# Performance work log

Measured on AMD Instinct MI355X. Metric: run time of the kernel, lower is better.

The kernel has to match this reference:

```python
import jax, jax.numpy as jnp
import numpy as np

GAMMA = 1.0

def _rbf_mean(a, b, gamma):
    # mean of exp(-gamma * ||a_i - b_j||^2) over the full [Na, Nb] kernel matrix
    aa = jnp.sum(a * a, axis=1, keepdims=True)          # [Na, 1]
    bb = jnp.sum(b * b, axis=1, keepdims=True)          # [Nb, 1]
    dist = aa + bb.T - 2.0 * (a @ b.T)                  # [Na, Nb]
    return jnp.mean(jnp.exp(-gamma * dist))

def setup_inputs() -> dict:
    key = jax.random.key(0)
    kx, ky = jax.random.split(key)
    N, D = 8192, 128
    x = jax.random.normal(kx, (N, D), dtype=jnp.float32)
    y = jax.random.normal(ky, (N, D), dtype=jnp.float32)
    return {"x": x, "y": y}

def reference(x, y):
    mmd = (_rbf_mean(x, x, GAMMA)
           + _rbf_mean(y, y, GAMMA)
           - 2.0 * _rbf_mean(x, y, GAMMA))
    return mmd
```

## Files before the change

### kernel.cpp

```cpp
#include <hip/hip_runtime.h>


#define N_PTS 8192
#define DCOLS 128
#define TILE 128
#define TJ 64
#define NSELF 2080
#define NJOBS 8256
#define NBLOCKS 512
#define LOG2E 1.4426950408889634f
#define THRESH -40.0f

typedef __attribute__((ext_vector_type(8))) short short8;
typedef __attribute__((ext_vector_type(4))) float floatx4;
typedef unsigned int u32;
typedef unsigned short u16;

#if __has_builtin(__builtin_amdgcn_exp2f)
#define EXP2(x) __builtin_amdgcn_exp2f(x)
#else
#define EXP2(x) exp2f(x)
#endif

__device__ __forceinline__ u16 f32_to_bf16(float f) {
  u32 u = __float_as_uint(f);
  u32 r = (u + 0x7fffu + ((u >> 16) & 1u)) >> 16;
  return (u16)r;
}

__device__ __forceinline__ void gl_lds16(const u16* g, u16* l) {
  __builtin_amdgcn_global_load_lds(
      (const __attribute__((address_space(1))) u32*)g,
      (__attribute__((address_space(3))) u32*)l, 16, 0, 0);
}

__global__ void prep_kernel(const float* __restrict__ x, const float* __restrict__ y,
                            u32* __restrict__ xb, u32* __restrict__ yb,
                            float* __restrict__ da, float* __restrict__ db,
                            u32* __restrict__ Sz) {
  if (blockIdx.x == 0 && threadIdx.x < 4) Sz[threadIdx.x] = 0;
  int wid = threadIdx.x >> 6;
  int lane = threadIdx.x & 63;
  int row = blockIdx.x * 4 + wid;
  const float* src;
  u32* dst;
  float* dn;
  int r;
  if (row < N_PTS) { src = x; dst = xb; dn = da; r = row; }
  else             { src = y; dst = yb; dn = db; r = row - N_PTS; }
  float2 v = ((const float2*)(src + (size_t)r * DCOLS))[lane];
  u16 b0 = f32_to_bf16(v.x), b1 = f32_to_bf16(v.y);
  float f0 = __uint_as_float((u32)b0 << 16);
  float f1 = __uint_as_float((u32)b1 << 16);
  float p = f0 * f0 + f1 * f1;
  dst[(size_t)r * 64 + lane] = (u32)b0 | ((u32)b1 << 16);
#pragma unroll
  for (int off = 32; off; off >>= 1) p += __shfl_down(p, off, 64);
  if (lane == 0) dn[r] = -LOG2E * p;
}

struct Job { int pair, rr, cc; };

__device__ __forceinline__ Job decode_job(int t) {
  Job jb;
  if (t < 2 * NSELF) {
    jb.pair = (t < NSELF) ? 0 : 1;
    int tt = t - jb.pair * NSELF;
    int r = 0;
    while (tt >= TJ - r) { tt -= TJ - r; r++; }
    jb.rr = r; jb.cc = r + tt;
  } else {
    int q = t - 2 * NSELF;
    jb.pair = 2; jb.rr = q >> 6; jb.cc = q & 63;
  }
  return jb;
}

__device__ __forceinline__ Job next_job(Job c) {
  Job n = c;
  if (c.pair == 2) {
    if (c.cc == 63) { n.rr++; n.cc = 0; } else n.cc++;
  } else {
    if (c.cc == 63) {
      if (c.rr == 63) { n.pair++; n.rr = 0; n.cc = 0; }
      else { n.rr++; n.cc = n.rr; }
    } else n.cc++;
  }
  return n;
}

__device__ __forceinline__ void pair_ptrs(int pair, const u16* xb, const u16* yb,
                                          const float* da, const float* db,
                                          const u16*& A, const u16*& B,
                                          const float*& dA, const float*& dB) {
  A = (pair == 1) ? yb : xb;
  B = (pair == 0) ? xb : yb;
  dA = (pair == 1) ? db : da;
  dB = (pair == 0) ? da : db;
}

__device__ __forceinline__ void stage_tile(const u16* gsrc, u16* ldst,
                                           int wid, int quad, int l15) {
#pragma unroll
  for (int i = 0; i < 8; i++) {
    int ch = wid * 8 + i;
    int lrow = ch * 4 + quad;
    int bsw = l15 ^ (lrow & 15);
    gl_lds16(gsrc + lrow * DCOLS + bsw * 8, ldst + ch * 512);
  }
}

__device__ __forceinline__ void load_afrags(const u16* gA, const float* gdA, int rr,
                                            int mbase, int quad, int l15,
                                            short8 afr[4][4], float dam[16]) {
  const u16* base = gA + (size_t)rr * (TILE * DCOLS);
#pragma unroll
  for (int ks = 0; ks < 4; ks++)
#pragma unroll
    for (int mi = 0; mi < 4; mi++)
      afr[ks][mi] = *(const short8*)(base + (mbase + mi * 16 + l15) * DCOLS +
                                     ks * 32 + quad * 8);
  const float* dr = gdA + rr * TILE + mbase;
#pragma unroll
  for (int mi = 0; mi < 4; mi++)
#pragma unroll
    for (int v = 0; v < 4; v++) dam[mi * 4 + v] = dr[mi * 16 + quad * 4 + v];
}

__global__ __launch_bounds__(256, 2) void mmd_kernel(
    const u16* __restrict__ xb, const u16* __restrict__ yb,
    const float* __restrict__ da, const float* __restrict__ db,
    float* __restrict__ S, u32* __restrict__ cnt, float* __restrict__ out) {
  __shared__ u16 Bt[2][TILE * DCOLS];

  int tid = threadIdx.x;
  int wid = tid >> 6, lane = tid & 63;
  int quad = lane >> 4, l15 = lane & 15;
  int mbase = (wid >> 1) * 64, nbase = (wid & 1) * 64;

  int start = (blockIdx.x * NJOBS) >> 9;
  int end = ((blockIdx.x + 1) * NJOBS) >> 9;

  Job cur = decode_job(start);
  const u16 *cA, *cB;
  const float *cdA, *cdB;
  pair_ptrs(cur.pair, xb, yb, da, db, cA, cB, cdA, cdB);

  short8 afr[4][4];
  float dam[16];
  load_afrags(cA, cdA, cur.rr, mbase, quad, l15, afr, dam);
  stage_tile(cB + (size_t)cur.cc * (TILE * DCOLS), &Bt[0][0], wid, quad, l15);
  __syncthreads();

  const float c1 = 2.0f * LOG2E;
  float tsum = 0.f;
  int p = 0;

  for (int j = start; j < end; j++) {
    bool hasNext = (j + 1 < end);
    Job nxt;
    const u16 *nA = cA, *nB = cB;
    const float *ndA = cdA, *ndB = cdB;

    float dbn[4];
    {
      const float* dr = cdB + cur.cc * TILE + nbase;
#pragma unroll
      for (int ni = 0; ni < 4; ni++) dbn[ni] = dr[ni * 16 + l15];
    }

    if (hasNext) {
      nxt = next_job(cur);
      pair_ptrs(nxt.pair, xb, yb, da, db, nA, nB, ndA, ndB);
      stage_tile(nB + (size_t)nxt.cc * (TILE * DCOLS), &Bt[p ^ 1][0], wid, quad, l15);
    }

    floatx4 acc[4][4];
    floatx4 zero = {0.f, 0.f, 0.f, 0.f};
#pragma unroll
    for (int mi = 0; mi < 4; mi++)
#pragma unroll
      for (int ni = 0; ni < 4; ni++) acc[mi][ni] = zero;

#pragma unroll
    for (int ks = 0; ks < 4; ks++) {
      short8 bf[4];
      int slot = (ks * 4 + quad) ^ l15;
#pragma unroll
      for (int ni = 0; ni < 4; ni++) {
        int row = nbase + ni * 16 + l15;
        bf[ni] = *(const short8*)(&Bt[p][row * DCOLS + slot * 8]);
      }
#pragma unroll
      for (int mi = 0; mi < 4; mi++)
#pragma unroll
        for (int ni = 0; ni < 4; ni++)
          acc[mi][ni] = __builtin_amdgcn_mfma_f32_16x16x32_bf16(
              afr[ks][mi], bf[ni], acc[mi][ni], 0, 0, 0);
    }

    float w = (cur.pair < 2 && cur.rr != cur.cc) ? 2.0f : 1.0f;
#pragma unroll
    for (int mi = 0; mi < 4; mi++) {
#pragma unroll
      for (int ni = 0; ni < 4; ni++) {
        float tv0 = fmaf(c1, acc[mi][ni][0], dam[mi * 4 + 0]);
        float tv1 = fmaf(c1, acc[mi][ni][1], dam[mi * 4 + 1]);
        float tv2 = fmaf(c1, acc[mi][ni][2], dam[mi * 4 + 2]);
        float tv3 = fmaf(c1, acc[mi][ni][3], dam[mi * 4 + 3]);
        float mx = fmaxf(fmaxf(tv0, tv1), fmaxf(tv2, tv3)) + dbn[ni];
        if (__any(mx > THRESH)) {
          float e = EXP2(tv0 + dbn[ni]) + EXP2(tv1 + dbn[ni]) +
                    EXP2(tv2 + dbn[ni]) + EXP2(tv3 + dbn[ni]);
          tsum = fmaf(w, e, tsum);
        }
      }
    }

    bool flush = !hasNext || (nxt.pair != cur.pair);
    if (flush) {
      float r = tsum;
#pragma unroll
      for (int off = 32; off; off >>= 1) r += __shfl_down(r, off, 64);
      if (lane == 0) atomicAdd(&S[cur.pair], r);
      tsum = 0.f;
    }

    if (hasNext && (nxt.pair != cur.pair || nxt.rr != cur.rr))
      load_afrags(nA, ndA, nxt.rr, mbase, quad, l15, afr, dam);

    __syncthreads();
    p ^= 1;
    if (hasNext) { cur = nxt; cA = nA; cB = nB; cdA = ndA; cdB = ndB; }
  }

  __syncthreads();
  if (tid == 0) {
    __threadfence();
    u32 old = atomicAdd(cnt, 1u);
    if (old == (u32)(NBLOCKS - 1)) {
      float s0 = atomicAdd(&S[0], 0.0f);
      float s1 = atomicAdd(&S[1], 0.0f);
      float s2 = atomicAdd(&S[2], 0.0f);
      out[0] = (s0 + s1 - 2.0f * s2) * (1.0f / ((float)N_PTS * (float)N_PTS));
    }
  }
}

extern "C" void kernel_launch(void* const* d_in, const int* in_sizes, int n_in,
                              void* d_out, int out_size, void* d_ws, size_t ws_size,
                              hipStream_t stream) {
  const float* x = (const float*)d_in[0];
  const float* y = (const float*)d_in[1];
  char* ws = (char*)d_ws;
  float* S = (float*)ws;
  u32* cnt = (u32*)ws + 3;
  u32* xb = (u32*)(ws + 256);
  u32* yb = (u32*)(ws + 256 + 2097152);
  float* da = (float*)(ws + 256 + 2 * 2097152);
  float* db = (float*)(ws + 256 + 2 * 2097152 + 32768);

  prep_kernel<<<4096, 256, 0, stream>>>(x, y, xb, yb, da, db, (u32*)ws);
  mmd_kernel<<<NBLOCKS, 256, 0, stream>>>((const u16*)xb, (const u16*)yb,
                                          da, db, S, cnt, (float*)d_out);
}
```

Measured before the change: 129.0 us.

## Switch to per-wave 64x64 tiles with 32x32 MFMA and register-streamed B

Each wave now owns an independent 64x64 output tile job, computed with 32x32x16 bf16 MFMA. B fragments stream straight from global memory into registers with a two-step lookahead, replacing the shared-memory staging and the block-wide barriers. The early-exit test now uses a row-max norm bound to skip tiles whose exponentials underflow, and the prep kernel processes 4 elements per lane. The aim is to remove LDS and sync overhead, but B is no longer reused across waves through LDS, so global and L2 traffic rises.

```diff
diff --git a/kernel.cpp b/kernel.cpp
--- a/kernel.cpp
+++ b/kernel.cpp
@@ -2,17 +2,16 @@
 
 
 #define N_PTS 8192
-#define DCOLS 128
-#define TILE 128
-#define TJ 64
-#define NSELF 2080
-#define NJOBS 8256
-#define NBLOCKS 512
+#define TJ 128
+#define NSELF 8256
+#define NT 32896
+#define NBLOCKS 1024
+#define NWAVES (NBLOCKS * 4)
 #define LOG2E 1.4426950408889634f
 #define THRESH -40.0f
 
 typedef __attribute__((ext_vector_type(8))) short short8;
-typedef __attribute__((ext_vector_type(4))) float floatx4;
+typedef __attribute__((ext_vector_type(16))) float floatx16;
 typedef unsigned int u32;
 typedef unsigned short u16;
 
@@ -28,38 +27,32 @@
   return (u16)r;
 }
 
-__device__ __forceinline__ void gl_lds16(const u16* g, u16* l) {
-  __builtin_amdgcn_global_load_lds(
-      (const __attribute__((address_space(1))) u32*)g,
-      (__attribute__((address_space(3))) u32*)l, 16, 0, 0);
-}
-
 __global__ void prep_kernel(const float* __restrict__ x, const float* __restrict__ y,
                             u32* __restrict__ xb, u32* __restrict__ yb,
                             float* __restrict__ da, float* __restrict__ db,
                             u32* __restrict__ Sz) {
   if (blockIdx.x == 0 && threadIdx.x < 4) Sz[threadIdx.x] = 0;
-  int wid = threadIdx.x >> 6;
-  int lane = threadIdx.x & 63;
-  int row = blockIdx.x * 4 + wid;
-  const float* src;
-  u32* dst;
-  float* dn;
-  int r;
+  int row = blockIdx.x * 8 + (threadIdx.x >> 5);
+  int l = threadIdx.x & 31;
+  const float* src; u32* dst; float* dn; int r;
   if (row < N_PTS) { src = x; dst = xb; dn = da; r = row; }
   else             { src = y; dst = yb; dn = db; r = row - N_PTS; }
-  float2 v = ((const float2*)(src + (size_t)r * DCOLS))[lane];
+  float4 v = ((const float4*)(src + (size_t)r * 128))[l];
   u16 b0 = f32_to_bf16(v.x), b1 = f32_to_bf16(v.y);
-  float f0 = __uint_as_float((u32)b0 << 16);
-  float f1 = __uint_as_float((u32)b1 << 16);
-  float p = f0 * f0 + f1 * f1;
-  dst[(size_t)r * 64 + lane] = (u32)b0 | ((u32)b1 << 16);
-#pragma unroll
-  for (int off = 32; off; off >>= 1) p += __shfl_down(p, off, 64);
-  if (lane == 0) dn[r] = -LOG2E * p;
-}
-
-struct Job { int pair, rr, cc; };
+  u16 b2 = f32_to_bf16(v.z), b3 = f32_to_bf16(v.w);
+  float f0 = __uint_as_float((u32)b0 << 16), f1 = __uint_as_float((u32)b1 << 16);
+  float f2 = __uint_as_float((u32)b2 << 16), f3 = __uint_as_float((u32)b3 << 16);
+  float p = f0 * f0 + f1 * f1 + f2 * f2 + f3 * f3;
+  uint2 pk;
+  pk.x = (u32)b0 | ((u32)b1 << 16);
+  pk.y = (u32)b2 | ((u32)b3 << 16);
+  ((uint2*)(dst + (size_t)r * 64))[l] = pk;
+#pragma unroll
+  for (int off = 16; off; off >>= 1) p += __shfl_xor(p, off, 64);
+  if (l == 0) dn[r] = -LOG2E * p;
+}
+
+struct Job { int pair, rb, cc; };
 
 __device__ __forceinline__ Job decode_job(int t) {
   Job jb;
@@ -68,177 +61,152 @@
     int tt = t - jb.pair * NSELF;
     int r = 0;
     while (tt >= TJ - r) { tt -= TJ - r; r++; }
-    jb.rr = r; jb.cc = r + tt;
+    jb.rb = r; jb.cc = r + tt;
   } else {
     int q = t - 2 * NSELF;
-    jb.pair = 2; jb.rr = q >> 6; jb.cc = q & 63;
+    jb.pair = 2; jb.rb = q >> 7; jb.cc = q & 127;
   }
   return jb;
 }
 
 __device__ __forceinline__ Job next_job(Job c) {
   Job n = c;
-  if (c.pair == 2) {
-    if (c.cc == 63) { n.rr++; n.cc = 0; } else n.cc++;
-  } else {
-    if (c.cc == 63) {
-      if (c.rr == 63) { n.pair++; n.rr = 0; n.cc = 0; }
-      else { n.rr++; n.cc = n.rr; }
-    } else n.cc++;
-  }
-  return n;
-}
-
-__device__ __forceinline__ void pair_ptrs(int pair, const u16* xb, const u16* yb,
-                                          const float* da, const float* db,
-                                          const u16*& A, const u16*& B,
-                                          const float*& dA, const float*& dB) {
-  A = (pair == 1) ? yb : xb;
-  B = (pair == 0) ? xb : yb;
-  dA = (pair == 1) ? db : da;
-  dB = (pair == 0) ? da : db;
-}
-
-__device__ __forceinline__ void stage_tile(const u16* gsrc, u16* ldst,
-                                           int wid, int quad, int l15) {
-#pragma unroll
-  for (int i = 0; i < 8; i++) {
-    int ch = wid * 8 + i;
-    int lrow = ch * 4 + quad;
-    int bsw = l15 ^ (lrow & 15);
-    gl_lds16(gsrc + lrow * DCOLS + bsw * 8, ldst + ch * 512);
-  }
-}
-
-__device__ __forceinline__ void load_afrags(const u16* gA, const float* gdA, int rr,
-                                            int mbase, int quad, int l15,
-                                            short8 afr[4][4], float dam[16]) {
-  const u16* base = gA + (size_t)rr * (TILE * DCOLS);
-#pragma unroll
-  for (int ks = 0; ks < 4; ks++)
-#pragma unroll
-    for (int mi = 0; mi < 4; mi++)
-      afr[ks][mi] = *(const short8*)(base + (mbase + mi * 16 + l15) * DCOLS +
-                                     ks * 32 + quad * 8);
-  const float* dr = gdA + rr * TILE + mbase;
-#pragma unroll
-  for (int mi = 0; mi < 4; mi++)
-#pragma unroll
-    for (int v = 0; v < 4; v++) dam[mi * 4 + v] = dr[mi * 16 + quad * 4 + v];
+  if (c.cc < TJ - 1) { n.cc++; return n; }
+  if (c.pair == 2) { n.rb++; n.cc = 0; return n; }
+  if (c.rb == TJ - 1) { n.pair = c.pair + 1; n.rb = 0; n.cc = 0; return n; }
+  n.rb = c.rb + 1; n.cc = n.rb; return n;
+}
+
+__device__ __forceinline__ const u16* selA(int p, const u16* xb, const u16* yb) {
+  return (p == 1) ? yb : xb;
+}
+__device__ __forceinline__ const u16* selB(int p, const u16* xb, const u16* yb) {
+  return (p == 0) ? xb : yb;
+}
+
+__device__ __forceinline__ void load_strip(const u16* A, const float* dA, int rb,
+                                           int l31, int h,
+                                           short8 afr[8][2], float damMax[2]) {
+#pragma unroll
+  for (int ks = 0; ks < 8; ks++)
+#pragma unroll
+    for (int mi = 0; mi < 2; mi++)
+      afr[ks][mi] = *(const short8*)(A + (size_t)(rb * 64 + mi * 32 + l31) * 128 +
+                                     ks * 16 + h * 8);
+#pragma unroll
+  for (int mi = 0; mi < 2; mi++) {
+    float v = dA[rb * 64 + mi * 32 + l31];
+#pragma unroll
+    for (int off = 16; off; off >>= 1) v = fmaxf(v, __shfl_xor(v, off, 64));
+    damMax[mi] = v;
+  }
 }
 
 __global__ __launch_bounds__(256, 2) void mmd_kernel(
     const u16* __restrict__ xb, const u16* __restrict__ yb,
     const float* __restrict__ da, const float* __restrict__ db,
     float* __restrict__ S, u32* __restrict__ cnt, float* __restrict__ out) {
-  __shared__ u16 Bt[2][TILE * DCOLS];
-
-  int tid = threadIdx.x;
-  int wid = tid >> 6, lane = tid & 63;
-  int quad = lane >> 4, l15 = lane & 15;
-  int mbase = (wid >> 1) * 64, nbase = (wid & 1) * 64;
-
-  int start = (blockIdx.x * NJOBS) >> 9;
-  int end = ((blockIdx.x + 1) * NJOBS) >> 9;
+  int g = blockIdx.x * 4 + (threadIdx.x >> 6);
+  int lane = threadIdx.x & 63;
+  int l31 = lane & 31, h = lane >> 5;
+
+  int start = (g * NT) >> 12;
+  int end = ((g + 1) * NT) >> 12;
 
   Job cur = decode_job(start);
-  const u16 *cA, *cB;
-  const float *cdA, *cdB;
-  pair_ptrs(cur.pair, xb, yb, da, db, cA, cB, cdA, cdB);
-
-  short8 afr[4][4];
-  float dam[16];
-  load_afrags(cA, cdA, cur.rr, mbase, quad, l15, afr, dam);
-  stage_tile(cB + (size_t)cur.cc * (TILE * DCOLS), &Bt[0][0], wid, quad, l15);
-  __syncthreads();
+  short8 afr[8][2];
+  float damMax[2];
+  load_strip(selA(cur.pair, xb, yb), (cur.pair == 1) ? db : da, cur.rb, l31, h,
+             afr, damMax);
+
+  int boff0 = l31 * 128 + h * 8;
+  int boff1 = (32 + l31) * 128 + h * 8;
+  const u16* Bt = selB(cur.pair, xb, yb) + (size_t)cur.cc * 8192;
+
+  short8 bf[4][2];
+  bf[0][0] = *(const short8*)(Bt + boff0);
+  bf[0][1] = *(const short8*)(Bt + boff1);
+  bf[1][0] = *(const short8*)(Bt + boff0 + 16);
+  bf[1][1] = *(const short8*)(Bt + boff1 + 16);
 
   const float c1 = 2.0f * LOG2E;
   float tsum = 0.f;
-  int p = 0;
 
   for (int j = start; j < end; j++) {
     bool hasNext = (j + 1 < end);
-    Job nxt;
-    const u16 *nA = cA, *nB = cB;
-    const float *ndA = cdA, *ndB = cdB;
-
-    float dbn[4];
+    Job nxt = cur;
+    if (hasNext) nxt = next_job(cur);
+    const u16* Bnxt = selB(nxt.pair, xb, yb) + (size_t)nxt.cc * 8192;
+
+    const float* dBc = (cur.pair == 0) ? da : db;
+    float dbn0 = dBc[cur.cc * 64 + l31];
+    float dbn1 = dBc[cur.cc * 64 + 32 + l31];
+
+    floatx16 acc00, acc01, acc10, acc11;
+#pragma unroll
+    for (int i = 0; i < 16; i++) { acc00[i] = 0.f; acc01[i] = 0.f; acc10[i] = 0.f; acc11[i] = 0.f; }
+
+#pragma unroll
+    for (int ks = 0; ks < 8; ks++) {
+      int s2 = (ks + 2) & 3;
+      if (ks < 6) {
+        bf[s2][0] = *(const short8*)(Bt + boff0 + (ks + 2) * 16);
+        bf[s2][1] = *(const short8*)(Bt + boff1 + (ks + 2) * 16);
+      } else if (hasNext) {
+        bf[s2][0] = *(const short8*)(Bnxt + boff0 + (ks - 6) * 16);
+        bf[s2][1] = *(const short8*)(Bnxt + boff1 + (ks - 6) * 16);
+      }
+      int s = ks & 3;
+      acc00 = __builtin_amdgcn_mfma_f32_32x32x16_bf16(afr[ks][0], bf[s][0], acc00, 0, 0, 0);
+      acc01 = __builtin_amdgcn_mfma_f32_32x32x16_bf16(afr[ks][0], bf[s][1], acc01, 0, 0, 0);
+      acc10 = __builtin_amdgcn_mfma_f32_32x32x16_bf16(afr[ks][1], bf[s][0], acc10, 0, 0, 0);
+      acc11 = __builtin_amdgcn_mfma_f32_32x32x16_bf16(afr[ks][1], bf[s][1], acc11, 0, 0, 0);
+    }
+
     {
-      const float* dr = cdB + cur.cc * TILE + nbase;
-#pragma unroll
-      for (int ni = 0; ni < 4; ni++) dbn[ni] = dr[ni * 16 + l15];
-    }
-
-    if (hasNext) {
-      nxt = next_job(cur);
-      pair_ptrs(nxt.pair, xb, yb, da, db, nA, nB, ndA, ndB);
-      stage_tile(nB + (size_t)nxt.cc * (TILE * DCOLS), &Bt[p ^ 1][0], wid, quad, l15);
-    }
-
-    floatx4 acc[4][4];
-    floatx4 zero = {0.f, 0.f, 0.f, 0.f};
-#pragma unroll
-    for (int mi = 0; mi < 4; mi++)
-#pragma unroll
-      for (int ni = 0; ni < 4; ni++) acc[mi][ni] = zero;
-
-#pragma unroll
-    for (int ks = 0; ks < 4; ks++) {
-      short8 bf[4];
-      int slot = (ks * 4 + quad) ^ l15;
-#pragma unroll
-      for (int ni = 0; ni < 4; ni++) {
-        int row = nbase + ni * 16 + l15;
-        bf[ni] = *(const short8*)(&Bt[p][row * DCOLS + slot * 8]);
+      float w = (cur.pair < 2 && cur.rb != cur.cc) ? 2.0f : 1.0f;
+      const float* dAc = (cur.pair == 1) ? db : da;
+#define DO_FRAG(A_, MI_, DBN_)                                                  \
+      {                                                                         \
+        float mx = (A_)[0];                                                     \
+        _Pragma("unroll")                                                       \
+        for (int i = 1; i < 16; i++) mx = fmaxf(mx, (A_)[i]);                   \
+        if (__any(fmaf(c1, mx, damMax[MI_] + (DBN_)) > THRESH)) {               \
+          int rbase = cur.rb * 64 + (MI_) * 32 + 4 * h;                         \
+          _Pragma("unroll")                                                     \
+          for (int r = 0; r < 16; r++) {                                        \
+            float dam = dAc[rbase + (r & 3) + 8 * (r >> 2)];                    \
+            tsum = fmaf(w, EXP2(fmaf(c1, (A_)[r], dam + (DBN_))), tsum);        \
+          }                                                                     \
+        }                                                                       \
       }
-#pragma unroll
-      for (int mi = 0; mi < 4; mi++)
-#pragma unroll
-        for (int ni = 0; ni < 4; ni++)
-          acc[mi][ni] = __builtin_amdgcn_mfma_f32_16x16x32_bf16(
-              afr[ks][mi], bf[ni], acc[mi][ni], 0, 0, 0);
-    }
-
-    float w = (cur.pair < 2 && cur.rr != cur.cc) ? 2.0f : 1.0f;
-#pragma unroll
-    for (int mi = 0; mi < 4; mi++) {
-#pragma unroll
-      for (int ni = 0; ni < 4; ni++) {
-        float tv0 = fmaf(c1, acc[mi][ni][0], dam[mi * 4 + 0]);
-        float tv1 = fmaf(c1, acc[mi][ni][1], dam[mi * 4 + 1]);
-        float tv2 = fmaf(c1, acc[mi][ni][2], dam[mi * 4 + 2]);
-        float tv3 = fmaf(c1, acc[mi][ni][3], dam[mi * 4 + 3]);
-        float mx = fmaxf(fmaxf(tv0, tv1), fmaxf(tv2, tv3)) + dbn[ni];
-        if (__any(mx > THRESH)) {
-          float e = EXP2(tv0 + dbn[ni]) + EXP2(tv1 + dbn[ni]) +
-                    EXP2(tv2 + dbn[ni]) + EXP2(tv3 + dbn[ni]);
-          tsum = fmaf(w, e, tsum);
-        }
-      }
-    }
-
-    bool flush = !hasNext || (nxt.pair != cur.pair);
-    if (flush) {
+      DO_FRAG(acc00, 0, dbn0)
+      DO_FRAG(acc01, 0, dbn1)
+      DO_FRAG(acc10, 1, dbn0)
+      DO_FRAG(acc11, 1, dbn1)
+#undef DO_FRAG
+    }
+
+    bool pairChange = hasNext && (nxt.pair != cur.pair);
+    if (!hasNext || pairChange) {
       float r = tsum;
 #pragma unroll
       for (int off = 32; off; off >>= 1) r += __shfl_down(r, off, 64);
       if (lane == 0) atomicAdd(&S[cur.pair], r);
       tsum = 0.f;
     }
-
-    if (hasNext && (nxt.pair != cur.pair || nxt.rr != cur.rr))
-      load_afrags(nA, ndA, nxt.rr, mbase, quad, l15, afr, dam);
-
-    __syncthreads();
-    p ^= 1;
-    if (hasNext) { cur = nxt; cA = nA; cB = nB; cdA = ndA; cdB = ndB; }
-  }
-
-  __syncthreads();
-  if (tid == 0) {
+    if (hasNext && (pairChange || nxt.rb != cur.rb))
+      load_strip(selA(nxt.pair, xb, yb), (nxt.pair == 1) ? db : da, nxt.rb,
+                 l31, h, afr, damMax);
+
+    Bt = Bnxt;
+    cur = nxt;
+  }
+
+  if (lane == 0) {
     __threadfence();
     u32 old = atomicAdd(cnt, 1u);
-    if (old == (u32)(NBLOCKS - 1)) {
+    if (old == (u32)(NWAVES - 1)) {
       float s0 = atomicAdd(&S[0], 0.0f);
       float s1 = atomicAdd(&S[1], 0.0f);
       float s2 = atomicAdd(&S[2], 0.0f);
@@ -260,7 +228,7 @@
   float* da = (float*)(ws + 256 + 2 * 2097152);
   float* db = (float*)(ws + 256 + 2 * 2097152 + 32768);
 
-  prep_kernel<<<4096, 256, 0, stream>>>(x, y, xb, yb, da, db, (u32*)ws);
+  prep_kernel<<<2048, 256, 0, stream>>>(x, y, xb, yb, da, db, (u32*)ws);
   mmd_kernel<<<NBLOCKS, 256, 0, stream>>>((const u16*)xb, (const u16*)yb,
                                           da, db, S, cnt, (float*)d_out);
 }
```

Result: slower. 223.0 us (+72.9%).
